# Performance work log

Hardware: AMD Instinct MI355X
Metric: run time of the kernel (lower is better)

Reference implementation:

```python
import jax, jax.numpy as jnp
import numpy as np
from jax import lax

EPS_ACT = 1e-5
EPS_RMS = 1e-6


def _ste(x, q):
    # straight-through estimator: forward = q, backward = identity
    return x + lax.stop_gradient(q - x)


def _act_quant8(x):
    # per-last-dim symmetric 8-bit activation quantization (BitNet style)
    scale = 127.0 / jnp.clip(jnp.max(jnp.abs(x), axis=-1, keepdims=True), EPS_ACT)
    return jnp.clip(jnp.round(x * scale), -128.0, 127.0) / scale


def _w_quant_8bit(w):
    # per-tensor symmetric 8-bit weight quantization
    scale = 127.0 / jnp.clip(jnp.max(jnp.abs(w)), EPS_ACT)
    return jnp.clip(jnp.round(w * scale), -128.0, 127.0) / scale


def _w_quant_binary(w):
    # per-tensor binary: sign(w) * mean(|w|)
    return jnp.sign(w) * jnp.mean(jnp.abs(w))


def _rmsnorm(x):
    return x * lax.rsqrt(jnp.mean(x * x, axis=-1, keepdims=True) + EPS_RMS)


def _bit_conv(x, w, quant_type, groups):
    xq = _ste(x, _act_quant8(x))
    wq = _ste(w, _w_quant_binary(w) if quant_type == 'Binary' else _w_quant_8bit(w))
    return lax.conv_general_dilated(
        xq, wq, window_strides=(1, 1), padding='VALID',
        feature_group_count=groups,
        dimension_numbers=('NCHW', 'OIHW', 'NCHW'))


def _bit_linear(x, w):
    x = _rmsnorm(x)                       # NormType='RMS' (no learned scale)
    xq = _ste(x, _act_quant8(x))
    wq = _ste(w, _w_quant_binary(w))      # QuantType='Binary', per-tensor
    return xq @ wq.T


def setup_inputs() -> dict:
    key = jax.random.key(0)
    ks = jax.random.split(key, 8)
    B = 8192
    return {
        'x':        jax.random.normal(ks[0], (B, 1, 16, 16), jnp.float32),
        'w_conv1':  jax.random.normal(ks[1], (16, 1, 3, 3),  jnp.float32) * 0.1,
        'w_conv1b': jax.random.normal(ks[2], (16, 16, 3, 3), jnp.float32) * 0.1,
        'w_conv2':  jax.random.normal(ks[3], (96, 1, 12, 12), jnp.float32) * 0.1,
        'w_fc1':    jax.random.normal(ks[4], (64, 96), jnp.float32) * 0.1,
        'w_fc2':    jax.random.normal(ks[5], (64, 64), jnp.float32) * 0.1,
        'w_fc3':    jax.random.normal(ks[6], (64, 64), jnp.float32) * 0.1,
        'w_fcl':    jax.random.normal(ks[7], (10, 64), jnp.float32) * 0.1,
    }


def reference(x, w_conv1, w_conv1b, w_conv2, w_fc1, w_fc2, w_fc3, w_fcl):
    h = jax.nn.relu(_bit_conv(x, w_conv1, '8bit', 1))        # [B,16,14,14]
    h = jax.nn.relu(_bit_conv(h, w_conv1b, '8bit', 1))       # [B,16,12,12]
    h = jax.nn.relu(_bit_conv(h, w_conv2, 'Binary', 16))     # [B,96,1,1]
    h = h.reshape(h.shape[0], -1)                            # [B,96]
    h = jax.nn.relu(_bit_linear(h, w_fc1))                   # [B,64]
    h = jax.nn.relu(_bit_linear(h, w_fc2))                   # [B,64]
    h = jax.nn.relu(_bit_linear(h, w_fc3))                   # [B,64]
    return _bit_linear(h, w_fcl)                             # [B,10]
```

## Files before the change

kernel.cpp:

```cpp
#include <hip/hip_runtime.h>
#include <math.h>


#define OFF_W1   0
#define OFF_W1B  192
#define OFF_W2   3264
#define OFF_F1   17088
#define OFF_F2   23232
#define OFF_F3   27328
#define OFF_FL   31424

#define EPS_TIE  3e-5f

__device__ __forceinline__ float quantq(float v, float s) {
    const float u  = __fmul_rn(v, s);
    const float fl = floorf(u);
    const float fr = __fsub_rn(u, fl);
    float q;
    if (fabsf(__fsub_rn(fr, 0.5f)) < EPS_TIE) q = __fadd_rn(fl, 0.5f);
    else                                      q = rintf(u);
    q = fminf(q, 127.f);
    return __fdiv_rn(q, s);
}

__device__ __forceinline__ float leaf_abs_sum(const float* __restrict__ p, int n) {
    float r[8];
    #pragma unroll
    for (int j = 0; j < 8; ++j) r[j] = fabsf(p[j]);
    const int nb = n & ~7;
    for (int i = 8; i < nb; i += 8) {
        #pragma unroll
        for (int j = 0; j < 8; ++j) r[j] = __fadd_rn(r[j], fabsf(p[i + j]));
    }
    float c = __fadd_rn(__fadd_rn(__fadd_rn(r[0], r[1]), __fadd_rn(r[2], r[3])),
                        __fadd_rn(__fadd_rn(r[4], r[5]), __fadd_rn(r[6], r[7])));
    for (int i = nb; i < n; ++i) c = __fadd_rn(c, fabsf(p[i]));
    return c;
}

__global__ __launch_bounds__(256) void wq_kernel(
    const float* __restrict__ w1, const float* __restrict__ w1b,
    const float* __restrict__ w2, const float* __restrict__ f1,
    const float* __restrict__ f2, const float* __restrict__ f3,
    const float* __restrict__ fl, float* __restrict__ ws)
{
    __shared__ float red[256];
    __shared__ float ls[128];
    const int blk = blockIdx.x, t = threadIdx.x;

    const float* src; int n; int mode; int off; int K; int W;
    switch (blk) {
        case 0:  src = w1;  n = 144;   mode = 0; off = OFF_W1;  K = 0;   W = 0;  break;
        case 1:  src = w1b; n = 2304;  mode = 0; off = OFF_W1B; K = 0;   W = 0;  break;
        case 2:  src = w2;  n = 13824; mode = 1; off = OFF_W2;  K = 144; W = 96; break;
        case 3:  src = f1;  n = 6144;  mode = 1; off = OFF_F1;  K = 96;  W = 64; break;
        case 4:  src = f2;  n = 4096;  mode = 1; off = OFF_F2;  K = 64;  W = 64; break;
        case 5:  src = f3;  n = 4096;  mode = 1; off = OFF_F3;  K = 64;  W = 64; break;
        default: src = fl;  n = 640;   mode = 1; off = OFF_FL;  K = 64;  W = 10; break;
    }

    if (mode == 0) {
        float p = 0.f;
        for (int i = t; i < n; i += 256) p = fmaxf(p, fabsf(src[i]));
        red[t] = p;
        __syncthreads();
        for (int s = 128; s > 0; s >>= 1) {
            if (t < s) red[t] = fmaxf(red[t], red[t + s]);
            __syncthreads();
        }
        const float s = __fdiv_rn(127.0f, fmaxf(red[0], 1e-5f));
        for (int i = t; i < n; i += 256) {
            float q = rintf(__fmul_rn(src[i], s));
            q = fminf(fmaxf(q, -128.f), 127.f);
            int d;
            if (blk == 0) d = (i / 9) * 12 + (i % 9);
            else          { const int oc = i / 144, k = i % 144;
                            d = oc * 192 + (k / 9) * 12 + (k % 9); }
            ws[off + d] = __fdiv_rn(q, s);
        }
    } else {
        int nleaf, loff, lsz;
        switch (n) {
            case 13824: nleaf = 128; loff = (t >> 1) * 216 + (t & 1) * 104;
                        lsz = (t & 1) ? 112 : 104; break;
            case 6144:  nleaf = 64;  loff = t * 96;  lsz = 96;  break;
            case 4096:  nleaf = 32;  loff = t * 128; lsz = 128; break;
            default:    nleaf = 8;   loff = t * 80;  lsz = 80;  break;
        }
        if (t < nleaf) ls[t] = leaf_abs_sum(src + loff, lsz);
        __syncthreads();
        for (int m = nleaf >> 1; m >= 1; m >>= 1) {
            float v = 0.f;
            if (t < m) v = __fadd_rn(ls[2 * t], ls[2 * t + 1]);
            __syncthreads();
            if (t < m) ls[t] = v;
            __syncthreads();
        }
        const float alpha = __fdiv_rn(ls[0], (float)n);
        for (int i = t; i < n; i += 256) {
            const float w = src[i];
            const float sg = (w > 0.f) ? 1.f : ((w < 0.f) ? -1.f : 0.f);
            const int d = (i % K) * W + (i / K);
            ws[off + d] = __fmul_rn(sg, alpha);
        }
    }
}

__global__ __launch_bounds__(256) void fused_kernel(
    const float* __restrict__ x, const float* __restrict__ ws,
    float* __restrict__ out)
{
    __shared__ __align__(16) float s_x[16][20];
    __shared__ __align__(16) float s_h1[16][14][20];
    __shared__ __align__(16) float s_h2[16][12][20];
    __shared__ float s_v96[96];
    __shared__ float s_t96[96];
    __shared__ float s_q[96];
    __shared__ float s_v64[64];
    __shared__ float s_r8[8];
    __shared__ float s_bc;

    const int b = blockIdx.x;
    const int t = threadIdx.x;

    {
        const float v = x[b * 256 + t];
        float m = fabsf(v);
        #pragma unroll
        for (int msk = 8; msk >= 1; msk >>= 1) m = fmaxf(m, __shfl_xor(m, msk, 16));
        const float s = __fdiv_rn(127.0f, fmaxf(m, 1e-5f));
        float q = rintf(__fmul_rn(v, s));
        q = fminf(fmaxf(q, -128.f), 127.f);
        s_x[t >> 4][t & 15] = __fdiv_rn(q, s);
    }
    __syncthreads();

    if (t < 224) {
        const int oc = t / 14, oh = t % 14;
        const float* __restrict__ wg = ws + OFF_W1 + oc * 12;
        const float4 wv0 = *(const float4*)&wg[0];
        const float4 wv1 = *(const float4*)&wg[4];
        const float  w8  = wg[8];
        const float w[9] = {wv0.x, wv0.y, wv0.z, wv0.w,
                            wv1.x, wv1.y, wv1.z, wv1.w, w8};
        float acc[14];
        #pragma unroll
        for (int ow = 0; ow < 14; ++ow) acc[ow] = 0.f;
        #pragma unroll
        for (int kh = 0; kh < 3; ++kh) {
            float A[16];
            #pragma unroll
            for (int j4 = 0; j4 < 4; ++j4)
                *(float4*)&A[j4 * 4] = *(const float4*)&s_x[oh + kh][j4 * 4];
            #pragma unroll
            for (int kw = 0; kw < 3; ++kw) {
                const float wk = w[kh * 3 + kw];
                #pragma unroll
                for (int ow = 0; ow < 14; ++ow)
                    acc[ow] = __fmaf_rn(A[ow + kw], wk, acc[ow]);
            }
        }
        float mx = 0.f;
        #pragma unroll
        for (int ow = 0; ow < 14; ++ow) { acc[ow] = fmaxf(acc[ow], 0.f); mx = fmaxf(mx, acc[ow]); }
        const float s = __fdiv_rn(127.0f, fmaxf(mx, 1e-5f));
        float q[14];
        #pragma unroll
        for (int ow = 0; ow < 14; ++ow) q[ow] = quantq(acc[ow], s);
        *(float4*)&s_h1[oc][oh][0]  = *(const float4*)&q[0];
        *(float4*)&s_h1[oc][oh][4]  = *(const float4*)&q[4];
        *(float4*)&s_h1[oc][oh][8]  = *(const float4*)&q[8];
        *(float2*)&s_h1[oc][oh][12] = *(const float2*)&q[12];
    }
    __syncthreads();

    if (t < 192) {
        const int oc = t / 12, oh = t % 12;
        const float* __restrict__ wg = ws + OFF_W1B + oc * 192;
        float acc[12];
        #pragma unroll
        for (int i = 0; i < 12; ++i) acc[i] = 0.f;
        for (int ic = 0; ic < 16; ++ic) {
            const float4 wv0 = *(const float4*)&wg[ic * 12];
            const float4 wv1 = *(const float4*)&wg[ic * 12 + 4];
            const float  w8  = wg[ic * 12 + 8];
            const float wr[9] = {wv0.x, wv0.y, wv0.z, wv0.w,
                                 wv1.x, wv1.y, wv1.z, wv1.w, w8};
            #pragma unroll
            for (int kh = 0; kh < 3; ++kh) {
                float A[14];
                *(float4*)&A[0]  = *(const float4*)&s_h1[ic][oh + kh][0];
                *(float4*)&A[4]  = *(const float4*)&s_h1[ic][oh + kh][4];
                *(float4*)&A[8]  = *(const float4*)&s_h1[ic][oh + kh][8];
                *(float2*)&A[12] = *(const float2*)&s_h1[ic][oh + kh][12];
                #pragma unroll
                for (int kw = 0; kw < 3; ++kw) {
                    const float w = wr[kh * 3 + kw];
                    #pragma unroll
                    for (int ow = 0; ow < 12; ++ow)
                        acc[ow] = __fmaf_rn(A[ow + kw], w, acc[ow]);
                }
            }
        }
        float mx = 0.f;
        #pragma unroll
        for (int ow = 0; ow < 12; ++ow) { acc[ow] = fmaxf(acc[ow], 0.f); mx = fmaxf(mx, acc[ow]); }
        const float s = __fdiv_rn(127.0f, fmaxf(mx, 1e-5f));
        float q[12];
        #pragma unroll
        for (int ow = 0; ow < 12; ++ow) q[ow] = quantq(acc[ow], s);
        *(float4*)&s_h2[oc][oh][0] = *(const float4*)&q[0];
        *(float4*)&s_h2[oc][oh][4] = *(const float4*)&q[4];
        *(float4*)&s_h2[oc][oh][8] = *(const float4*)&q[8];
    }
    __syncthreads();

    if (t < 96) {
        const int g = t / 6;
        const float* __restrict__ wp = ws + OFF_W2;
        float acc = 0.f;
        #pragma unroll
        for (int r = 0; r < 12; ++r) {
            float A[12];
            *(float4*)&A[0] = *(const float4*)&s_h2[g][r][0];
            *(float4*)&A[4] = *(const float4*)&s_h2[g][r][4];
            *(float4*)&A[8] = *(const float4*)&s_h2[g][r][8];
            #pragma unroll
            for (int c = 0; c < 12; ++c)
                acc = __fmaf_rn(A[c], wp[(r * 12 + c) * 96 + t], acc);
        }
        s_v96[t] = fmaxf(acc, 0.f);
    }
    __syncthreads();

    if (t < 96) s_t96[t] = __fmul_rn(s_v96[t], s_v96[t]);
    __syncthreads();
    if (t < 8) {
        float r = s_t96[t];
        for (int i = 8; i < 96; i += 8) r = __fadd_rn(r, s_t96[i + t]);
        s_r8[t] = r;
    }
    __syncthreads();
    if (t == 0) {
        const float c = __fadd_rn(
            __fadd_rn(__fadd_rn(s_r8[0], s_r8[1]), __fadd_rn(s_r8[2], s_r8[3])),
            __fadd_rn(__fadd_rn(s_r8[4], s_r8[5]), __fadd_rn(s_r8[6], s_r8[7])));
        const float mean = __fdiv_rn(c, 96.0f);
        s_bc = __fdiv_rn(1.0f, __fsqrt_rn(__fadd_rn(mean, 1e-6f)));
    }
    __syncthreads();
    if (t < 96) s_t96[t] = __fmul_rn(s_v96[t], s_bc);
    __syncthreads();
    if (t < 64) {
        float m = s_t96[t];
        if (t < 32) m = fmaxf(m, s_t96[64 + t]);
        #pragma unroll
        for (int msk = 32; msk >= 1; msk >>= 1) m = fmaxf(m, __shfl_xor(m, msk, 64));
        if (t == 0) s_bc = __fdiv_rn(127.0f, fmaxf(m, 1e-5f));
    }
    __syncthreads();
    if (t < 96) s_q[t] = quantq(s_t96[t], s_bc);
    __syncthreads();
    if (t < 64) {
        const float* __restrict__ wp = ws + OFF_F1;
        float acc = 0.f;
        for (int k = 0; k < 96; ++k) acc = __fmaf_rn(s_q[k], wp[k * 64 + t], acc);
        s_v64[t] = fmaxf(acc, 0.f);
    }
    __syncthreads();

    #pragma unroll 1
    for (int stage = 0; stage < 2; ++stage) {
        const int woff = stage == 0 ? OFF_F2 : OFF_F3;
        if (t < 64) s_t96[t] = __fmul_rn(s_v64[t], s_v64[t]);
        __syncthreads();
        if (t < 8) {
            float r = s_t96[t];
            for (int i = 8; i < 64; i += 8) r = __fadd_rn(r, s_t96[i + t]);
            s_r8[t] = r;
        }
        __syncthreads();
        if (t == 0) {
            const float c = __fadd_rn(
                __fadd_rn(__fadd_rn(s_r8[0], s_r8[1]), __fadd_rn(s_r8[2], s_r8[3])),
                __fadd_rn(__fadd_rn(s_r8[4], s_r8[5]), __fadd_rn(s_r8[6], s_r8[7])));
            const float mean = __fdiv_rn(c, 64.0f);
            s_bc = __fdiv_rn(1.0f, __fsqrt_rn(__fadd_rn(mean, 1e-6f)));
        }
        __syncthreads();
        if (t < 64) s_t96[t] = __fmul_rn(s_v64[t], s_bc);
        __syncthreads();
        if (t < 64) {
            float m = s_t96[t];
            #pragma unroll
            for (int msk = 32; msk >= 1; msk >>= 1) m = fmaxf(m, __shfl_xor(m, msk, 64));
            if (t == 0) s_bc = __fdiv_rn(127.0f, fmaxf(m, 1e-5f));
        }
        __syncthreads();
        if (t < 64) s_q[t] = quantq(s_t96[t], s_bc);
        __syncthreads();
        if (t < 64) {
            const float* __restrict__ wp = ws + woff;
            float acc = 0.f;
            for (int k = 0; k < 64; ++k) acc = __fmaf_rn(s_q[k], wp[k * 64 + t], acc);
            s_v64[t] = fmaxf(acc, 0.f);
        }
        __syncthreads();
    }

    if (t < 64) s_t96[t] = __fmul_rn(s_v64[t], s_v64[t]);
    __syncthreads();
    if (t < 8) {
        float r = s_t96[t];
        for (int i = 8; i < 64; i += 8) r = __fadd_rn(r, s_t96[i + t]);
        s_r8[t] = r;
    }
    __syncthreads();
    if (t == 0) {
        const float c = __fadd_rn(
            __fadd_rn(__fadd_rn(s_r8[0], s_r8[1]), __fadd_rn(s_r8[2], s_r8[3])),
            __fadd_rn(__fadd_rn(s_r8[4], s_r8[5]), __fadd_rn(s_r8[6], s_r8[7])));
        const float mean = __fdiv_rn(c, 64.0f);
        s_bc = __fdiv_rn(1.0f, __fsqrt_rn(__fadd_rn(mean, 1e-6f)));
    }
    __syncthreads();
    if (t < 64) s_t96[t] = __fmul_rn(s_v64[t], s_bc);
    __syncthreads();
    if (t < 64) {
        float m = s_t96[t];
        #pragma unroll
        for (int msk = 32; msk >= 1; msk >>= 1) m = fmaxf(m, __shfl_xor(m, msk, 64));
        if (t == 0) s_bc = __fdiv_rn(127.0f, fmaxf(m, 1e-5f));
    }
    __syncthreads();
    if (t < 64) s_q[t] = quantq(s_t96[t], s_bc);
    __syncthreads();
    if (t < 10) {
        const float* __restrict__ wp = ws + OFF_FL;
        float acc = 0.f;
        for (int k = 0; k < 64; ++k) acc = __fmaf_rn(s_q[k], wp[k * 10 + t], acc);
        out[b * 10 + t] = acc;
    }
}

extern "C" void kernel_launch(void* const* d_in, const int* in_sizes, int n_in,
                              void* d_out, int out_size, void* d_ws, size_t ws_size,
                              hipStream_t stream) {
    const float* x   = (const float*)d_in[0];
    const float* w1  = (const float*)d_in[1];
    const float* w1b = (const float*)d_in[2];
    const float* w2  = (const float*)d_in[3];
    const float* f1  = (const float*)d_in[4];
    const float* f2  = (const float*)d_in[5];
    const float* f3  = (const float*)d_in[6];
    const float* fl  = (const float*)d_in[7];
    float* out = (float*)d_out;
    float* ws  = (float*)d_ws;

    const int B = in_sizes[0] / 256;

    wq_kernel<<<7, 256, 0, stream>>>(w1, w1b, w2, f1, f2, f3, fl, ws);
    fused_kernel<<<B, 256, 0, stream>>>(x, ws, out);
}
```

Before: 264.4 us.

## Use packed FP32 FMA in convs and drop barriers in single-wave FC tail

Rewrites the two 3x3 conv inner loops around v_pk_fma_f32 inline asm, so pairs of output columns accumulate in one instruction. The odd-offset middle tap stays on scalar FMAs. After conv2, all threads except the first 64 exit. The RMSNorm, quantisation and FC chain then runs in one wavefront, with the __syncthreads barriers and single-thread broadcasts replaced by per-lane computation and shuffles. It also pads the h2 LDS channel stride to 244 to reduce bank conflicts and adds a min-blocks-per-CU launch bound of 4, which may raise register pressure or cause spills. Dropping the barriers relies on LDS ordering within a wave.

```diff
diff --git a/kernel.cpp b/kernel.cpp
--- a/kernel.cpp
+++ b/kernel.cpp
@@ -11,6 +11,12 @@
 #define OFF_FL   31424
 
 #define EPS_TIE  3e-5f
+
+typedef float f32x2 __attribute__((ext_vector_type(2)));
+
+__device__ __forceinline__ void pk_fma(f32x2& acc, f32x2 a, f32x2 w) {
+    asm("v_pk_fma_f32 %0, %1, %2, %0" : "+v"(acc) : "v"(a), "v"(w));
+}
 
 __device__ __forceinline__ float quantq(float v, float s) {
     const float u  = __fmul_rn(v, s);
@@ -106,19 +112,19 @@
     }
 }
 
-__global__ __launch_bounds__(256) void fused_kernel(
+#define H2S 244
+
+__global__ __launch_bounds__(256, 4) void fused_kernel(
     const float* __restrict__ x, const float* __restrict__ ws,
     float* __restrict__ out)
 {
     __shared__ __align__(16) float s_x[16][20];
     __shared__ __align__(16) float s_h1[16][14][20];
-    __shared__ __align__(16) float s_h2[16][12][20];
+    __shared__ __align__(16) float s_h2f[16 * H2S];
     __shared__ float s_v96[96];
     __shared__ float s_t96[96];
     __shared__ float s_q[96];
-    __shared__ float s_v64[64];
     __shared__ float s_r8[8];
-    __shared__ float s_bc;
 
     const int b = blockIdx.x;
     const int t = threadIdx.x;
@@ -141,25 +147,40 @@
         const float4 wv0 = *(const float4*)&wg[0];
         const float4 wv1 = *(const float4*)&wg[4];
         const float  w8  = wg[8];
-        const float w[9] = {wv0.x, wv0.y, wv0.z, wv0.w,
-                            wv1.x, wv1.y, wv1.z, wv1.w, w8};
-        float acc[14];
-        #pragma unroll
-        for (int ow = 0; ow < 14; ++ow) acc[ow] = 0.f;
+        const float wr[9] = {wv0.x, wv0.y, wv0.z, wv0.w,
+                             wv1.x, wv1.y, wv1.z, wv1.w, w8};
+        f32x2 acc2[7];
+        #pragma unroll
+        for (int j = 0; j < 7; ++j) { acc2[j][0] = 0.f; acc2[j][1] = 0.f; }
         #pragma unroll
         for (int kh = 0; kh < 3; ++kh) {
             float A[16];
-            #pragma unroll
-            for (int j4 = 0; j4 < 4; ++j4)
-                *(float4*)&A[j4 * 4] = *(const float4*)&s_x[oh + kh][j4 * 4];
-            #pragma unroll
-            for (int kw = 0; kw < 3; ++kw) {
-                const float wk = w[kh * 3 + kw];
-                #pragma unroll
-                for (int ow = 0; ow < 14; ++ow)
-                    acc[ow] = __fmaf_rn(A[ow + kw], wk, acc[ow]);
+            *(float4*)&A[0]  = *(const float4*)&s_x[oh + kh][0];
+            *(float4*)&A[4]  = *(const float4*)&s_x[oh + kh][4];
+            *(float4*)&A[8]  = *(const float4*)&s_x[oh + kh][8];
+            *(float4*)&A[12] = *(const float4*)&s_x[oh + kh][12];
+            const float w0 = wr[kh * 3 + 0], w1k = wr[kh * 3 + 1], w2k = wr[kh * 3 + 2];
+            f32x2 wp0; wp0[0] = w0;  wp0[1] = w0;
+            f32x2 wp2; wp2[0] = w2k; wp2[1] = w2k;
+            #pragma unroll
+            for (int j = 0; j < 7; ++j) {
+                f32x2 a; a[0] = A[2 * j]; a[1] = A[2 * j + 1];
+                pk_fma(acc2[j], a, wp0);
             }
-        }
+            #pragma unroll
+            for (int j = 0; j < 7; ++j) {
+                acc2[j][0] = __fmaf_rn(A[2 * j + 1], w1k, acc2[j][0]);
+                acc2[j][1] = __fmaf_rn(A[2 * j + 2], w1k, acc2[j][1]);
+            }
+            #pragma unroll
+            for (int j = 0; j < 7; ++j) {
+                f32x2 a; a[0] = A[2 * j + 2]; a[1] = A[2 * j + 3];
+                pk_fma(acc2[j], a, wp2);
+            }
+        }
+        float acc[14];
+        #pragma unroll
+        for (int j = 0; j < 7; ++j) { acc[2 * j] = acc2[j][0]; acc[2 * j + 1] = acc2[j][1]; }
         float mx = 0.f;
         #pragma unroll
         for (int ow = 0; ow < 14; ++ow) { acc[ow] = fmaxf(acc[ow], 0.f); mx = fmaxf(mx, acc[ow]); }
@@ -177,9 +198,10 @@
     if (t < 192) {
         const int oc = t / 12, oh = t % 12;
         const float* __restrict__ wg = ws + OFF_W1B + oc * 192;
-        float acc[12];
-        #pragma unroll
-        for (int i = 0; i < 12; ++i) acc[i] = 0.f;
+        f32x2 acc2[6];
+        #pragma unroll
+        for (int j = 0; j < 6; ++j) { acc2[j][0] = 0.f; acc2[j][1] = 0.f; }
+        #pragma unroll 2
         for (int ic = 0; ic < 16; ++ic) {
             const float4 wv0 = *(const float4*)&wg[ic * 12];
             const float4 wv1 = *(const float4*)&wg[ic * 12 + 4];
@@ -193,15 +215,29 @@
                 *(float4*)&A[4]  = *(const float4*)&s_h1[ic][oh + kh][4];
                 *(float4*)&A[8]  = *(const float4*)&s_h1[ic][oh + kh][8];
                 *(float2*)&A[12] = *(const float2*)&s_h1[ic][oh + kh][12];
+                const float w0 = wr[kh * 3 + 0], w1k = wr[kh * 3 + 1], w2k = wr[kh * 3 + 2];
+                f32x2 wp0; wp0[0] = w0;  wp0[1] = w0;
+                f32x2 wp2; wp2[0] = w2k; wp2[1] = w2k;
                 #pragma unroll
-                for (int kw = 0; kw < 3; ++kw) {
-                    const float w = wr[kh * 3 + kw];
-                    #pragma unroll
-                    for (int ow = 0; ow < 12; ++ow)
-                        acc[ow] = __fmaf_rn(A[ow + kw], w, acc[ow]);
+                for (int j = 0; j < 6; ++j) {
+                    f32x2 a; a[0] = A[2 * j]; a[1] = A[2 * j + 1];
+                    pk_fma(acc2[j], a, wp0);
+                }
+                #pragma unroll
+                for (int j = 0; j < 6; ++j) {
+                    acc2[j][0] = __fmaf_rn(A[2 * j + 1], w1k, acc2[j][0]);
+                    acc2[j][1] = __fmaf_rn(A[2 * j + 2], w1k, acc2[j][1]);
+                }
+                #pragma unroll
+                for (int j = 0; j < 6; ++j) {
+                    f32x2 a; a[0] = A[2 * j + 2]; a[1] = A[2 * j + 3];
+                    pk_fma(acc2[j], a, wp2);
                 }
             }
         }
+        float acc[12];
+        #pragma unroll
+        for (int j = 0; j < 6; ++j) { acc[2 * j] = acc2[j][0]; acc[2 * j + 1] = acc2[j][1]; }
         float mx = 0.f;
         #pragma unroll
         for (int ow = 0; ow < 12; ++ow) { acc[ow] = fmaxf(acc[ow], 0.f); mx = fmaxf(mx, acc[ow]); }
@@ -209,9 +245,9 @@
         float q[12];
         #pragma unroll
         for (int ow = 0; ow < 12; ++ow) q[ow] = quantq(acc[ow], s);
-        *(float4*)&s_h2[oc][oh][0] = *(const float4*)&q[0];
-        *(float4*)&s_h2[oc][oh][4] = *(const float4*)&q[4];
-        *(float4*)&s_h2[oc][oh][8] = *(const float4*)&q[8];
+        *(float4*)&s_h2f[oc * H2S + oh * 20 + 0] = *(const float4*)&q[0];
+        *(float4*)&s_h2f[oc * H2S + oh * 20 + 4] = *(const float4*)&q[4];
+        *(float4*)&s_h2f[oc * H2S + oh * 20 + 8] = *(const float4*)&q[8];
     }
     __syncthreads();
 
@@ -222,9 +258,9 @@
         #pragma unroll
         for (int r = 0; r < 12; ++r) {
             float A[12];
-            *(float4*)&A[0] = *(const float4*)&s_h2[g][r][0];
-            *(float4*)&A[4] = *(const float4*)&s_h2[g][r][4];
-            *(float4*)&A[8] = *(const float4*)&s_h2[g][r][8];
+            *(float4*)&A[0] = *(const float4*)&s_h2f[g * H2S + r * 20 + 0];
+            *(float4*)&A[4] = *(const float4*)&s_h2f[g * H2S + r * 20 + 4];
+            *(float4*)&A[8] = *(const float4*)&s_h2f[g * H2S + r * 20 + 8];
             #pragma unroll
             for (int c = 0; c < 12; ++c)
                 acc = __fmaf_rn(A[c], wp[(r * 12 + c) * 96 + t], acc);
@@ -233,113 +269,88 @@
     }
     __syncthreads();
 
-    if (t < 96) s_t96[t] = __fmul_rn(s_v96[t], s_v96[t]);
-    __syncthreads();
-    if (t < 8) {
-        float r = s_t96[t];
-        for (int i = 8; i < 96; i += 8) r = __fadd_rn(r, s_t96[i + t]);
-        s_r8[t] = r;
-    }
-    __syncthreads();
-    if (t == 0) {
+    if (t >= 64) return;
+
+    float u;
+    {
+        const float va = s_v96[t];
+        const float vb = (t < 32) ? s_v96[64 + t] : 0.f;
+        s_t96[t] = __fmul_rn(va, va);
+        if (t < 32) s_t96[64 + t] = __fmul_rn(vb, vb);
+        if (t < 8) {
+            float r = s_t96[t];
+            for (int i = 8; i < 96; i += 8) r = __fadd_rn(r, s_t96[i + t]);
+            s_r8[t] = r;
+        }
         const float c = __fadd_rn(
             __fadd_rn(__fadd_rn(s_r8[0], s_r8[1]), __fadd_rn(s_r8[2], s_r8[3])),
             __fadd_rn(__fadd_rn(s_r8[4], s_r8[5]), __fadd_rn(s_r8[6], s_r8[7])));
         const float mean = __fdiv_rn(c, 96.0f);
-        s_bc = __fdiv_rn(1.0f, __fsqrt_rn(__fadd_rn(mean, 1e-6f)));
-    }
-    __syncthreads();
-    if (t < 96) s_t96[t] = __fmul_rn(s_v96[t], s_bc);
-    __syncthreads();
-    if (t < 64) {
-        float m = s_t96[t];
-        if (t < 32) m = fmaxf(m, s_t96[64 + t]);
+        const float bc1 = __fdiv_rn(1.0f, __fsqrt_rn(__fadd_rn(mean, 1e-6f)));
+        const float n0 = __fmul_rn(va, bc1);
+        const float n1 = __fmul_rn(vb, bc1);
+        float m = n0;
+        if (t < 32) m = fmaxf(m, n1);
         #pragma unroll
         for (int msk = 32; msk >= 1; msk >>= 1) m = fmaxf(m, __shfl_xor(m, msk, 64));
-        if (t == 0) s_bc = __fdiv_rn(127.0f, fmaxf(m, 1e-5f));
-    }
-    __syncthreads();
-    if (t < 96) s_q[t] = quantq(s_t96[t], s_bc);
-    __syncthreads();
-    if (t < 64) {
+        const float s2 = __fdiv_rn(127.0f, fmaxf(m, 1e-5f));
+        s_q[t] = quantq(n0, s2);
+        if (t < 32) s_q[64 + t] = quantq(n1, s2);
         const float* __restrict__ wp = ws + OFF_F1;
         float acc = 0.f;
         for (int k = 0; k < 96; ++k) acc = __fmaf_rn(s_q[k], wp[k * 64 + t], acc);
-        s_v64[t] = fmaxf(acc, 0.f);
-    }
-    __syncthreads();
+        u = fmaxf(acc, 0.f);
+    }
 
     #pragma unroll 1
     for (int stage = 0; stage < 2; ++stage) {
         const int woff = stage == 0 ? OFF_F2 : OFF_F3;
-        if (t < 64) s_t96[t] = __fmul_rn(s_v64[t], s_v64[t]);
-        __syncthreads();
+        s_t96[t] = __fmul_rn(u, u);
         if (t < 8) {
             float r = s_t96[t];
             for (int i = 8; i < 64; i += 8) r = __fadd_rn(r, s_t96[i + t]);
             s_r8[t] = r;
         }
-        __syncthreads();
-        if (t == 0) {
-            const float c = __fadd_rn(
-                __fadd_rn(__fadd_rn(s_r8[0], s_r8[1]), __fadd_rn(s_r8[2], s_r8[3])),
-                __fadd_rn(__fadd_rn(s_r8[4], s_r8[5]), __fadd_rn(s_r8[6], s_r8[7])));
-            const float mean = __fdiv_rn(c, 64.0f);
-            s_bc = __fdiv_rn(1.0f, __fsqrt_rn(__fadd_rn(mean, 1e-6f)));
-        }
-        __syncthreads();
-        if (t < 64) s_t96[t] = __fmul_rn(s_v64[t], s_bc);
-        __syncthreads();
-        if (t < 64) {
-            float m = s_t96[t];
-            #pragma unroll
-            for (int msk = 32; msk >= 1; msk >>= 1) m = fmaxf(m, __shfl_xor(m, msk, 64));
-            if (t == 0) s_bc = __fdiv_rn(127.0f, fmaxf(m, 1e-5f));
-        }
-        __syncthreads();
-        if (t < 64) s_q[t] = quantq(s_t96[t], s_bc);
-        __syncthreads();
-        if (t < 64) {
-            const float* __restrict__ wp = ws + woff;
-            float acc = 0.f;
-            for (int k = 0; k < 64; ++k) acc = __fmaf_rn(s_q[k], wp[k * 64 + t], acc);
-            s_v64[t] = fmaxf(acc, 0.f);
-        }
-        __syncthreads();
-    }
-
-    if (t < 64) s_t96[t] = __fmul_rn(s_v64[t], s_v64[t]);
-    __syncthreads();
-    if (t < 8) {
-        float r = s_t96[t];
-        for (int i = 8; i < 64; i += 8) r = __fadd_rn(r, s_t96[i + t]);
-        s_r8[t] = r;
-    }
-    __syncthreads();
-    if (t == 0) {
         const float c = __fadd_rn(
             __fadd_rn(__fadd_rn(s_r8[0], s_r8[1]), __fadd_rn(s_r8[2], s_r8[3])),
             __fadd_rn(__fadd_rn(s_r8[4], s_r8[5]), __fadd_rn(s_r8[6], s_r8[7])));
         const float mean = __fdiv_rn(c, 64.0f);
-        s_bc = __fdiv_rn(1.0f, __fsqrt_rn(__fadd_rn(mean, 1e-6f)));
-    }
-    __syncthreads();
-    if (t < 64) s_t96[t] = __fmul_rn(s_v64[t], s_bc);
-    __syncthreads();
-    if (t < 64) {
-        float m = s_t96[t];
+        const float bc1 = __fdiv_rn(1.0f, __fsqrt_rn(__fadd_rn(mean, 1e-6f)));
+        const float n0 = __fmul_rn(u, bc1);
+        float m = n0;
         #pragma unroll
         for (int msk = 32; msk >= 1; msk >>= 1) m = fmaxf(m, __shfl_xor(m, msk, 64));
-        if (t == 0) s_bc = __fdiv_rn(127.0f, fmaxf(m, 1e-5f));
-    }
-    __syncthreads();
-    if (t < 64) s_q[t] = quantq(s_t96[t], s_bc);
-    __syncthreads();
-    if (t < 10) {
+        const float s2 = __fdiv_rn(127.0f, fmaxf(m, 1e-5f));
+        s_q[t] = quantq(n0, s2);
+        const float* __restrict__ wp = ws + woff;
+        float acc = 0.f;
+        for (int k = 0; k < 64; ++k) acc = __fmaf_rn(s_q[k], wp[k * 64 + t], acc);
+        u = fmaxf(acc, 0.f);
+    }
+
+    {
+        s_t96[t] = __fmul_rn(u, u);
+        if (t < 8) {
+            float r = s_t96[t];
+            for (int i = 8; i < 64; i += 8) r = __fadd_rn(r, s_t96[i + t]);
+            s_r8[t] = r;
+        }
+        const float c = __fadd_rn(
+            __fadd_rn(__fadd_rn(s_r8[0], s_r8[1]), __fadd_rn(s_r8[2], s_r8[3])),
+            __fadd_rn(__fadd_rn(s_r8[4], s_r8[5]), __fadd_rn(s_r8[6], s_r8[7])));
+        const float mean = __fdiv_rn(c, 64.0f);
+        const float bc1 = __fdiv_rn(1.0f, __fsqrt_rn(__fadd_rn(mean, 1e-6f)));
+        const float n0 = __fmul_rn(u, bc1);
+        float m = n0;
+        #pragma unroll
+        for (int msk = 32; msk >= 1; msk >>= 1) m = fmaxf(m, __shfl_xor(m, msk, 64));
+        const float s2 = __fdiv_rn(127.0f, fmaxf(m, 1e-5f));
+        s_q[t] = quantq(n0, s2);
+        const int to = (t < 10) ? t : 9;
         const float* __restrict__ wp = ws + OFF_FL;
         float acc = 0.f;
-        for (int k = 0; k < 64; ++k) acc = __fmaf_rn(s_q[k], wp[k * 10 + t], acc);
-        out[b * 10 + t] = acc;
+        for (int k = 0; k < 64; ++k) acc = __fmaf_rn(s_q[k], wp[k * 10 + to], acc);
+        if (t < 10) out[b * 10 + t] = acc;
     }
 }
 
```

New measurement: 277.5 us. 5.0% more time.
